# Kernel optimization log

Measured on AMD Instinct MI355X. Metric: run time of the kernel, lower is better.

The kernel has to match this reference:

```python
import jax, jax.numpy as jnp
import numpy as np

B, LQ, LK, D, H = 8, 512, 512, 512, 128

def setup_inputs() -> dict:
    key = jax.random.key(0)
    k1, k2, k3, k4, k5 = jax.random.split(key, 5)
    qs = jax.random.normal(k1, (B, LQ, D), dtype=jnp.float32)
    ks = jax.random.normal(k2, (B, LK, D), dtype=jnp.float32)
    # Dense kernels: flax Dense stores kernel as [in_features, out_features]
    Wq = jax.random.normal(k3, (D, H), dtype=jnp.float32) / np.sqrt(D)
    Wk = jax.random.normal(k4, (D, H), dtype=jnp.float32) / np.sqrt(D)
    wv = jax.random.normal(k5, (H,), dtype=jnp.float32) / np.sqrt(H)
    return {"qs": qs, "ks": ks, "Wq": Wq, "Wk": Wk, "wv": wv}

def reference(qs, ks, Wq, Wk, wv):
    # Project queries and keys into the shared hidden space: [B,Lq,H], [B,Lk,H]
    q = jnp.einsum("bqd,dh->bqh", qs, Wq)
    k = jnp.einsum("bkd,dh->bkh", ks, Wk)
    # Broadcast-add -> tanh -> linear reduce over H: scores [B,Lq,Lk]
    feats = jnp.tanh(q[:, :, None, :] + k[:, None, :, :])  # [B,Lq,Lk,H]
    return jnp.einsum("bqkh,h->bqk", feats, wv)
```

## Files before the change

### kernel.cpp

```cpp
#include <hip/hip_runtime.h>
#include <hip/hip_bf16.h>
#include <cstdint>

#define B_   8
#define LQ_  512
#define LK_  512
#define D_   512
#define H_   128

typedef __attribute__((ext_vector_type(8))) short  short8;
typedef __attribute__((ext_vector_type(4))) float  float4v;

#define TANH_C 2.8853900817779268f

__device__ __forceinline__ short bf16rne(float x) {
  uint32_t u = __float_as_uint(x);
  return (short)((u + 0x7fffu + ((u >> 16) & 1u)) >> 16);
}

__global__ __launch_bounds__(256) void prep_kernel(
    const float* __restrict__ Wq, const float* __restrict__ Wk,
    const float* __restrict__ wv,
    short* __restrict__ WqF, short* __restrict__ WkF,
    float* __restrict__ w2, float* __restrict__ W0buf) {
  int g = blockIdx.x * 256 + threadIdx.x;
  if (blockIdx.x == 0) {
    int t = threadIdx.x;
    if (t < H_) w2[t] = -2.0f * wv[t];
    if (t == H_) {
      float s = 0.f;
      for (int h = 0; h < H_; ++h) s += wv[h];
      W0buf[0] = s;
    }
  }
  int m = g >> 13;
  int r = g & 8191;
  int l  = r & 63;
  int kb = (r >> 6) & 15;
  int nt = r >> 10;
  int col = nt * 16 + (l & 15);
  int k0  = kb * 32 + ((l >> 4) << 3);
  const float* W = m ? Wk : Wq;
  short8 f;
#pragma unroll
  for (int j = 0; j < 8; ++j) f[j] = bf16rne(W[(k0 + j) * H_ + col]);
  ((short8*)(m ? WkF : WqF))[r] = f;
}

__global__ __launch_bounds__(256) void proj_kernel(
    const float* __restrict__ qs, const float* __restrict__ ks,
    const short* __restrict__ WqF, const short* __restrict__ WkF,
    float* __restrict__ qp, float* __restrict__ kp) {
  int blk  = blockIdx.x;
  int wave = threadIdx.x >> 6;
  int l    = threadIdx.x & 63;
  int grow = blk * 16;
  int m    = (grow >= 4096) ? 1 : 0;
  int r0   = grow - (m ? 4096 : 0);
  const float*  A  = m ? ks : qs;
  const short8* BF = (const short8*)(m ? WkF : WqF);
  float* out = m ? kp : qp;

  float4v acc[2];
  acc[0] = (float4v){0.f, 0.f, 0.f, 0.f};
  acc[1] = (float4v){0.f, 0.f, 0.f, 0.f};

  int quad = l >> 4;
  int arow = r0 + (l & 15);
  const float* aptr = A + (size_t)arow * D_ + quad * 8;
  int t0 = wave * 2;

#pragma unroll 4
  for (int kb = 0; kb < 16; ++kb) {
    float4v a0 = *(const float4v*)(aptr + kb * 32);
    float4v a1 = *(const float4v*)(aptr + kb * 32 + 4);
    short8 af;
#pragma unroll
    for (int j = 0; j < 4; ++j) { af[j] = bf16rne(a0[j]); af[j + 4] = bf16rne(a1[j]); }
#pragma unroll
    for (int tt = 0; tt < 2; ++tt) {
      short8 bf = BF[((t0 + tt) * 16 + kb) * 64 + l];
      acc[tt] = __builtin_amdgcn_mfma_f32_16x16x32_bf16(af, bf, acc[tt], 0, 0, 0);
    }
  }

#pragma unroll
  for (int tt = 0; tt < 2; ++tt)
#pragma unroll
    for (int r = 0; r < 4; ++r) {
      int row = r0 + quad * 4 + r;
      int col = (t0 + tt) * 16 + (l & 15);
      out[(size_t)row * H_ + col] = __builtin_amdgcn_exp2f(acc[tt][r] * TANH_C);
    }
}

__global__ __launch_bounds__(256) void score_kernel(
    const float* __restrict__ qp, const float* __restrict__ kp,
    const float* __restrict__ w2, const float* __restrict__ W0buf,
    float* __restrict__ out) {
  __shared__ float qt[32 * 68];
  __shared__ float kt[32 * 68];
  __shared__ float wl[H_];

  int b = blockIdx.z, qtile = blockIdx.y, ktile = blockIdx.x;
  int t = threadIdx.x;
  int tx = t & 15, ty = t >> 4;

  const float* qbase = qp + (size_t)(b * LQ_ + qtile * 32) * H_;
  const float* kbase = kp + (size_t)(b * LK_ + ktile * 32) * H_;

  float W0 = W0buf[0];

  if (t < 32) *(float4v*)&wl[t * 4] = *(const float4v*)&w2[t * 4];

  float accs[2][2];
  const float4v ones = (float4v){1.f, 1.f, 1.f, 1.f};
#pragma unroll
  for (int i = 0; i < 2; ++i)
#pragma unroll
    for (int j = 0; j < 2; ++j) accs[i][j] = 0.f;

  int lr = t >> 4, lc = t & 15;

  for (int hc = 0; hc < 2; ++hc) {
    __syncthreads();
#pragma unroll
    for (int s = 0; s < 2; ++s) {
      int row = lr + 16 * s;
      *(float4v*)&qt[row * 68 + lc * 4] =
          *(const float4v*)&qbase[row * H_ + hc * 64 + lc * 4];
      *(float4v*)&kt[row * 68 + lc * 4] =
          *(const float4v*)&kbase[row * H_ + hc * 64 + lc * 4];
    }
    __syncthreads();

#pragma unroll
    for (int h0 = 0; h0 < 64; h0 += 4) {
      float4v qv[2], kv[2];
#pragma unroll
      for (int i = 0; i < 2; ++i) qv[i] = *(const float4v*)&qt[(ty + 16 * i) * 68 + h0];
#pragma unroll
      for (int j = 0; j < 2; ++j) kv[j] = *(const float4v*)&kt[(tx + 16 * j) * 68 + h0];
      float4v w4 = *(const float4v*)&wl[hc * 64 + h0];

#pragma unroll
      for (int i = 0; i < 2; ++i)
#pragma unroll
        for (int j = 0; j < 2; ++j) {
          float4v den = __builtin_elementwise_fma(qv[i], kv[j], ones);
          float d01 = den[0] * den[1];
          float d23 = den[2] * den[3];
          float n01 = fmaf(w4[1], den[0], w4[0] * den[1]);
          float n23 = fmaf(w4[3], den[2], w4[2] * den[3]);
          float big = fmaf(n01, d23, n23 * d01);
          float r   = __builtin_amdgcn_rcpf(d01 * d23);
          accs[i][j] = fmaf(big, r, accs[i][j]);
        }
    }
  }

  size_t ob = (size_t)(b * LQ_ + qtile * 32) * LK_ + ktile * 32;
#pragma unroll
  for (int i = 0; i < 2; ++i)
#pragma unroll
    for (int j = 0; j < 2; ++j)
      out[ob + (size_t)(ty + 16 * i) * LK_ + tx + 16 * j] = W0 + accs[i][j];
}

extern "C" void kernel_launch(void* const* d_in, const int* in_sizes, int n_in,
                              void* d_out, int out_size, void* d_ws, size_t ws_size,
                              hipStream_t stream) {
  const float* qs = (const float*)d_in[0];
  const float* ks = (const float*)d_in[1];
  const float* Wq = (const float*)d_in[2];
  const float* Wk = (const float*)d_in[3];
  const float* wv = (const float*)d_in[4];
  float* out = (float*)d_out;

  char* ws = (char*)d_ws;
  short* WqF  = (short*)ws;
  short* WkF  = (short*)(ws + (128 << 10));
  float* qp   = (float*)(ws + (256 << 10));
  float* kp   = (float*)(ws + (256 << 10) + (2 << 20));
  float* w2   = (float*)(ws + (256 << 10) + (4 << 20));
  float* W0b  = (float*)(ws + (256 << 10) + (4 << 20) + 512);

  prep_kernel<<<64, 256, 0, stream>>>(Wq, Wk, wv, WqF, WkF, w2, W0b);
  proj_kernel<<<512, 256, 0, stream>>>(qs, ks, WqF, WkF, qp, kp);
  score_kernel<<<dim3(16, 16, 8), 256, 0, stream>>>(qp, kp, w2, W0b, out);
}
```

Baseline: 109.0 us.

## Enlarge score tile to 64x64 per block and split projection columns across blocks

The score kernel now computes a 64x64 output tile per block, with 4x4 results per thread instead of 2x2. This raises the arithmetic done per LDS load of the projected q/k vectors and quarters the number of blocks (512 instead of 2048). The projection kernel now gives each wave a single 16-column tile and launches twice as many blocks, which adds parallelism there. The trade-offs are higher register pressure and more LDS per block in the score kernel, plus fewer blocks to cover the 256 CUs.

Result: slower. 116.5 us (+6.8%).

```diff
diff --git a/kernel.cpp b/kernel.cpp
--- a/kernel.cpp
+++ b/kernel.cpp
@@ -54,21 +54,20 @@
   int blk  = blockIdx.x;
   int wave = threadIdx.x >> 6;
   int l    = threadIdx.x & 63;
-  int grow = blk * 16;
+  int rt   = blk >> 1;
+  int ct   = (blk & 1) * 4 + wave;
+  int grow = rt * 16;
   int m    = (grow >= 4096) ? 1 : 0;
   int r0   = grow - (m ? 4096 : 0);
   const float*  A  = m ? ks : qs;
   const short8* BF = (const short8*)(m ? WkF : WqF);
   float* out = m ? kp : qp;
 
-  float4v acc[2];
-  acc[0] = (float4v){0.f, 0.f, 0.f, 0.f};
-  acc[1] = (float4v){0.f, 0.f, 0.f, 0.f};
+  float4v acc = (float4v){0.f, 0.f, 0.f, 0.f};
 
   int quad = l >> 4;
   int arow = r0 + (l & 15);
   const float* aptr = A + (size_t)arow * D_ + quad * 8;
-  int t0 = wave * 2;
 
 #pragma unroll 4
   for (int kb = 0; kb < 16; ++kb) {
@@ -77,55 +76,50 @@
     short8 af;
 #pragma unroll
     for (int j = 0; j < 4; ++j) { af[j] = bf16rne(a0[j]); af[j + 4] = bf16rne(a1[j]); }
-#pragma unroll
-    for (int tt = 0; tt < 2; ++tt) {
-      short8 bf = BF[((t0 + tt) * 16 + kb) * 64 + l];
-      acc[tt] = __builtin_amdgcn_mfma_f32_16x16x32_bf16(af, bf, acc[tt], 0, 0, 0);
-    }
+    short8 bf = BF[(ct * 16 + kb) * 64 + l];
+    acc = __builtin_amdgcn_mfma_f32_16x16x32_bf16(af, bf, acc, 0, 0, 0);
   }
 
 #pragma unroll
-  for (int tt = 0; tt < 2; ++tt)
-#pragma unroll
-    for (int r = 0; r < 4; ++r) {
-      int row = r0 + quad * 4 + r;
-      int col = (t0 + tt) * 16 + (l & 15);
-      out[(size_t)row * H_ + col] = __builtin_amdgcn_exp2f(acc[tt][r] * TANH_C);
-    }
+  for (int r = 0; r < 4; ++r) {
+    int row = r0 + quad * 4 + r;
+    int col = ct * 16 + (l & 15);
+    out[(size_t)row * H_ + col] = __builtin_amdgcn_exp2f(acc[r] * TANH_C);
+  }
 }
 
 __global__ __launch_bounds__(256) void score_kernel(
     const float* __restrict__ qp, const float* __restrict__ kp,
     const float* __restrict__ w2, const float* __restrict__ W0buf,
     float* __restrict__ out) {
-  __shared__ float qt[32 * 68];
-  __shared__ float kt[32 * 68];
+  __shared__ float qt[64 * 68];
+  __shared__ float kt[64 * 68];
   __shared__ float wl[H_];
 
   int b = blockIdx.z, qtile = blockIdx.y, ktile = blockIdx.x;
   int t = threadIdx.x;
   int tx = t & 15, ty = t >> 4;
 
-  const float* qbase = qp + (size_t)(b * LQ_ + qtile * 32) * H_;
-  const float* kbase = kp + (size_t)(b * LK_ + ktile * 32) * H_;
+  const float* qbase = qp + (size_t)(b * LQ_ + qtile * 64) * H_;
+  const float* kbase = kp + (size_t)(b * LK_ + ktile * 64) * H_;
 
   float W0 = W0buf[0];
 
   if (t < 32) *(float4v*)&wl[t * 4] = *(const float4v*)&w2[t * 4];
 
-  float accs[2][2];
+  float accs[4][4];
   const float4v ones = (float4v){1.f, 1.f, 1.f, 1.f};
 #pragma unroll
-  for (int i = 0; i < 2; ++i)
+  for (int i = 0; i < 4; ++i)
 #pragma unroll
-    for (int j = 0; j < 2; ++j) accs[i][j] = 0.f;
+    for (int j = 0; j < 4; ++j) accs[i][j] = 0.f;
 
   int lr = t >> 4, lc = t & 15;
 
   for (int hc = 0; hc < 2; ++hc) {
     __syncthreads();
 #pragma unroll
-    for (int s = 0; s < 2; ++s) {
+    for (int s = 0; s < 4; ++s) {
       int row = lr + 16 * s;
       *(float4v*)&qt[row * 68 + lc * 4] =
           *(const float4v*)&qbase[row * H_ + hc * 64 + lc * 4];
@@ -134,19 +128,21 @@
     }
     __syncthreads();
 
+#pragma unroll 2
+    for (int h0 = 0; h0 < 64; h0 += 4) {
+      float4v qv[4], kv[4];
 #pragma unroll
-    for (int h0 = 0; h0 < 64; h0 += 4) {
-      float4v qv[2], kv[2];
+      for (int i = 0; i < 4; ++i)
+        qv[i] = *(const float4v*)&qt[(ty + 16 * i) * 68 + h0];
 #pragma unroll
-      for (int i = 0; i < 2; ++i) qv[i] = *(const float4v*)&qt[(ty + 16 * i) * 68 + h0];
-#pragma unroll
-      for (int j = 0; j < 2; ++j) kv[j] = *(const float4v*)&kt[(tx + 16 * j) * 68 + h0];
+      for (int j = 0; j < 4; ++j)
+        kv[j] = *(const float4v*)&kt[(tx + 16 * j) * 68 + h0];
       float4v w4 = *(const float4v*)&wl[hc * 64 + h0];
 
 #pragma unroll
-      for (int i = 0; i < 2; ++i)
+      for (int i = 0; i < 4; ++i)
 #pragma unroll
-        for (int j = 0; j < 2; ++j) {
+        for (int j = 0; j < 4; ++j) {
           float4v den = __builtin_elementwise_fma(qv[i], kv[j], ones);
           float d01 = den[0] * den[1];
           float d23 = den[2] * den[3];
@@ -159,11 +155,11 @@
     }
   }
 
-  size_t ob = (size_t)(b * LQ_ + qtile * 32) * LK_ + ktile * 32;
+  size_t ob = (size_t)(b * LQ_ + qtile * 64) * LK_ + ktile * 64;
 #pragma unroll
-  for (int i = 0; i < 2; ++i)
+  for (int i = 0; i < 4; ++i)
 #pragma unroll
-    for (int j = 0; j < 2; ++j)
+    for (int j = 0; j < 4; ++j)
       out[ob + (size_t)(ty + 16 * i) * LK_ + tx + 16 * j] = W0 + accs[i][j];
 }
 
@@ -186,6 +182,6 @@
   float* W0b  = (float*)(ws + (256 << 10) + (4 << 20) + 512);
 
   prep_kernel<<<64, 256, 0, stream>>>(Wq, Wk, wv, WqF, WkF, w2, W0b);
-  proj_kernel<<<512, 256, 0, stream>>>(qs, ks, WqF, WkF, qp, kp);
-  score_kernel<<<dim3(16, 16, 8), 256, 0, stream>>>(qp, kp, w2, W0b, out);
+  proj_kernel<<<1024, 256, 0, stream>>>(qs, ks, WqF, WkF, qp, kp);
+  score_kernel<<<dim3(8, 8, 8), 256, 0, stream>>>(qp, kp, w2, W0b, out);
 }
```
